# Performance work log

Hardware: AMD Instinct MI355X
Metric: run time of the kernel (lower is better)

## Reference

```python
import jax, jax.numpy as jnp
import numpy as np

B, C, FH, FW = 8, 256, 64, 64   # sketch/ref feature maps (B, C, F_H, F_W)
N = 131072                       # ~B*FH*FW*4 triplets, as the nested loops produce
MARGIN = 12.0


def setup_inputs() -> dict:
    key = jax.random.key(0)
    k1, k2, k3, k4, k5, k6 = jax.random.split(key, 6)
    sketch_query_vectors = jax.random.normal(k1, (B, C, FH, FW), jnp.float32)
    ref_key_vectors = jax.random.normal(k2, (B, C, FH, FW), jnp.float32)
    # Precomputed triplet indices. In the original these come from GridProcessing
    # (CPU grid math on G + random.choices negatives); they are constants w.r.t.
    # the float inputs, so we sample them once here.
    batch_idx = jax.random.randint(k3, (N,), 0, B, jnp.int32)
    anchor_yx = jax.random.randint(k4, (N, 2), 0, FH, jnp.int32)
    pos_yx = jax.random.randint(k5, (N, 2), 0, FH, jnp.int32)
    neg_yx = jax.random.randint(k6, (N, 2), 0, FH, jnp.int32)
    return {
        "sketch_query_vectors": sketch_query_vectors,
        "ref_key_vectors": ref_key_vectors,
        "batch_idx": batch_idx,
        "anchor_yx": anchor_yx,
        "pos_yx": pos_yx,
        "neg_yx": neg_yx,
    }


def reference(sketch_query_vectors, ref_key_vectors, batch_idx, anchor_yx, pos_yx, neg_yx):
    # Gather per-triplet feature vectors: [N, C]
    a = sketch_query_vectors[batch_idx, :, anchor_yx[:, 0], anchor_yx[:, 1]]
    p = ref_key_vectors[batch_idx, :, pos_yx[:, 0], pos_yx[:, 1]]
    n = ref_key_vectors[batch_idx, :, neg_yx[:, 0], neg_yx[:, 1]]
    dp = jnp.sum((a - p) ** 2, axis=-1)  # squared-euclidean, as calc_euclidean
    dn = jnp.sum((a - n) ** 2, axis=-1)
    losses = jax.nn.relu(dp - dn + MARGIN)  # per-triplet hinge (1-elem mean in orig)
    return jnp.sum(losses) / (1e-6 + N)
```

## Files before the change

### kernel.cpp

```cpp
#include <hip/hip_runtime.h>

#define NB 8
#define NC 256
#define FH 64
#define FW 64
#define NS (FH * FW)
#define NSAMP 131072
#define MARGIN_F 12.0f
#define GATHER_BLOCKS (NSAMP / 32)

typedef float vfloat2 __attribute__((ext_vector_type(2)));

__device__ __forceinline__ unsigned pack4_fp8(float f0, float f1, float f2, float f3)
{
    int r = __builtin_amdgcn_cvt_pk_fp8_f32(f0, f1, 0, false);
    r     = __builtin_amdgcn_cvt_pk_fp8_f32(f2, f3, r, true);
    return (unsigned)r;
}

__global__ __launch_bounds__(256) void transpose_to_bsc_fp8(
    const float* __restrict__ in0, const float* __restrict__ in1,
    unsigned char* __restrict__ out0, unsigned char* __restrict__ out1)
{
    __shared__ float tile[64][65];

    const int which = blockIdx.z >> 3;
    const int b     = blockIdx.z & 7;
    const float* __restrict__ in  = which ? in1 : in0;
    unsigned char* __restrict__ out = which ? out1 : out0;

    const int s0 = blockIdx.x * 64;
    const int c0 = blockIdx.y * 64;
    const int t  = threadIdx.x;

    const float* __restrict__ inb  = in  + (size_t)b * NC * NS;
    unsigned char* __restrict__ outb = out + (size_t)b * NS * NC;

    const int g   = t >> 4;
    const int sl4 = (t & 15) << 2;
#pragma unroll
    for (int pass = 0; pass < 4; ++pass) {
        const int cl = pass * 16 + g;
        const float4 v = *(const float4*)&inb[(size_t)(c0 + cl) * NS + (s0 + sl4)];
        tile[sl4 + 0][cl] = v.x;
        tile[sl4 + 1][cl] = v.y;
        tile[sl4 + 2][cl] = v.z;
        tile[sl4 + 3][cl] = v.w;
    }
    __syncthreads();

    const int cl4 = (t & 15) << 2;
#pragma unroll
    for (int pass = 0; pass < 4; ++pass) {
        const int sl = pass * 16 + (t >> 4);
        const unsigned w = pack4_fp8(tile[sl][cl4 + 0], tile[sl][cl4 + 1],
                                     tile[sl][cl4 + 2], tile[sl][cl4 + 3]);
        *(unsigned*)&outb[(size_t)(s0 + sl) * NC + (c0 + cl4)] = w;
    }
}

__device__ __forceinline__ void acc_u32(unsigned a, unsigned p, unsigned n, float& d)
{
    const vfloat2 a0 = __builtin_amdgcn_cvt_pk_f32_fp8(a, false);
    const vfloat2 a1 = __builtin_amdgcn_cvt_pk_f32_fp8(a, true);
    const vfloat2 p0 = __builtin_amdgcn_cvt_pk_f32_fp8(p, false);
    const vfloat2 p1 = __builtin_amdgcn_cvt_pk_f32_fp8(p, true);
    const vfloat2 n0 = __builtin_amdgcn_cvt_pk_f32_fp8(n, false);
    const vfloat2 n1 = __builtin_amdgcn_cvt_pk_f32_fp8(n, true);
    float t;
    t = a0.x - p0.x; d += t * t;  t = a0.x - n0.x; d -= t * t;
    t = a0.y - p0.y; d += t * t;  t = a0.y - n0.y; d -= t * t;
    t = a1.x - p1.x; d += t * t;  t = a1.x - n1.x; d -= t * t;
    t = a1.y - p1.y; d += t * t;  t = a1.y - n1.y; d -= t * t;
}

__device__ __forceinline__ void acc_quad(uint4 a, uint4 p, uint4 n, float& d)
{
    acc_u32(a.x, p.x, n.x, d);
    acc_u32(a.y, p.y, n.y, d);
    acc_u32(a.z, p.z, n.z, d);
    acc_u32(a.w, p.w, n.w, d);
}

__global__ __launch_bounds__(256) void triplet_gather_fp8(
    const uint4* __restrict__ tq,
    const uint4* __restrict__ tk,
    const int*  __restrict__ batch_idx,
    const int2* __restrict__ anchor_yx,
    const int2* __restrict__ pos_yx,
    const int2* __restrict__ neg_yx,
    float* __restrict__ partials)
{
    const int t    = threadIdx.x;
    const int ol   = t & 7;
    const int oct  = t >> 3;
    const int samp = blockIdx.x * 32 + oct;

    const int  b  = batch_idx[samp];
    const int2 ay = anchor_yx[samp];
    const int2 py = pos_yx[samp];
    const int2 ny = neg_yx[samp];

    const size_t ab = ((size_t)(b * NS) + ay.x * FW + ay.y) * 16;
    const size_t pb = ((size_t)(b * NS) + py.x * FW + py.y) * 16;
    const size_t nb = ((size_t)(b * NS) + ny.x * FW + ny.y) * 16;

    const uint4 A0 = tq[ab + ol];
    const uint4 A1 = tq[ab + 8 + ol];
    const uint4 P0 = tk[pb + ol];
    const uint4 P1 = tk[pb + 8 + ol];
    const uint4 N0 = tk[nb + ol];
    const uint4 N1 = tk[nb + 8 + ol];

    float d = 0.0f;
    acc_quad(A0, P0, N0, d);
    acc_quad(A1, P1, N1, d);

#pragma unroll
    for (int m = 1; m < 8; m <<= 1) d += __shfl_xor(d, m, 64);

    __shared__ float part[32];
    if (ol == 0) part[oct] = fmaxf(d + MARGIN_F, 0.0f);
    __syncthreads();
    if (t == 0) {
        float s = 0.0f;
#pragma unroll
        for (int i = 0; i < 32; ++i) s += part[i];
        partials[blockIdx.x] = s;
    }
}

__global__ __launch_bounds__(256) void final_reduce(
    const float* __restrict__ partials, float* __restrict__ out)
{
    float s = 0.0f;
    for (int i = threadIdx.x; i < GATHER_BLOCKS; i += 256) s += partials[i];
#pragma unroll
    for (int m = 1; m < 64; m <<= 1) s += __shfl_xor(s, m, 64);
    __shared__ float ws4[4];
    if ((threadIdx.x & 63) == 0) ws4[threadIdx.x >> 6] = s;
    __syncthreads();
    if (threadIdx.x == 0) {
        const float invN = 1.0f / (1e-6f + (float)NSAMP);
        out[0] = (ws4[0] + ws4[1] + ws4[2] + ws4[3]) * invN;
    }
}

__global__ __launch_bounds__(256) void triplet_direct(
    const float* __restrict__ q, const float* __restrict__ k,
    const int*  __restrict__ batch_idx,
    const int2* __restrict__ anchor_yx,
    const int2* __restrict__ pos_yx,
    const int2* __restrict__ neg_yx,
    float* __restrict__ out)
{
    const int lane   = threadIdx.x & 63;
    const int wid    = threadIdx.x >> 6;
    const int gwave  = blockIdx.x * 4 + wid;
    const int nwaves = gridDim.x * 4;

    float wsum = 0.0f;
    for (int i = gwave; i < NSAMP; i += nwaves) {
        const int  b  = batch_idx[i];
        const int2 ay = anchor_yx[i];
        const int2 py = pos_yx[i];
        const int2 ny = neg_yx[i];

        const size_t base = (size_t)b * NC * NS;
        const int sa = ay.x * FW + ay.y;
        const int sp = py.x * FW + py.y;
        const int sn = ny.x * FW + ny.y;

        float d = 0.0f;
#pragma unroll
        for (int kk = 0; kk < 4; ++kk) {
            const int c = lane + 64 * kk;
            const float av = q[base + (size_t)c * NS + sa];
            const float pv = k[base + (size_t)c * NS + sp];
            const float nv = k[base + (size_t)c * NS + sn];
            float t;
            t = av - pv; d += t * t;
            t = av - nv; d -= t * t;
        }
#pragma unroll
        for (int m = 1; m < 64; m <<= 1) d += __shfl_xor(d, m, 64);
        if (lane == 0) wsum += fmaxf(d + MARGIN_F, 0.0f);
    }

    __shared__ float bsum[4];
    if (lane == 0) bsum[wid] = wsum;
    __syncthreads();
    if (threadIdx.x == 0) {
        const float invN = 1.0f / (1e-6f + (float)NSAMP);
        atomicAdd(out, (bsum[0] + bsum[1] + bsum[2] + bsum[3]) * invN);
    }
}

extern "C" void kernel_launch(void* const* d_in, const int* in_sizes, int n_in,
                              void* d_out, int out_size, void* d_ws, size_t ws_size,
                              hipStream_t stream)
{
    const float* sketch = (const float*)d_in[0];
    const float* refk   = (const float*)d_in[1];
    const int*   bidx   = (const int*)d_in[2];
    const int2*  ayx    = (const int2*)d_in[3];
    const int2*  pyx    = (const int2*)d_in[4];
    const int2*  nyx    = (const int2*)d_in[5];
    float*       out    = (float*)d_out;

    const size_t tensor_elems = (size_t)NB * NC * NS;
    const size_t need = 2 * tensor_elems * sizeof(unsigned char)
                      + GATHER_BLOCKS * sizeof(float);

    if (ws_size >= need) {
        unsigned char* tq = (unsigned char*)d_ws;
        unsigned char* tk = tq + tensor_elems;
        float* partials = (float*)(tk + tensor_elems);

        dim3 tgrid(NS / 64, NC / 64, 16);
        transpose_to_bsc_fp8<<<tgrid, 256, 0, stream>>>(sketch, refk, tq, tk);

        triplet_gather_fp8<<<GATHER_BLOCKS, 256, 0, stream>>>(
            (const uint4*)tq, (const uint4*)tk, bidx, ayx, pyx, nyx, partials);

        final_reduce<<<1, 256, 0, stream>>>(partials, out);
    } else {
        (void)hipMemsetAsync(out, 0, sizeof(float), stream);
        triplet_direct<<<4096, 256, 0, stream>>>(
            sketch, refk, bidx, ayx, pyx, nyx, out);
    }
}
```

Baseline: 121.7 us.

## Bin gather samples by batch per block, flatten transpose grid, drop reduce kernel

The gather kernel now splits each window of 256 samples across 8 blocks. Each block is pinned to one batch index and compacts the samples of that batch with ballot and popcount, so every block touches only one batch slice of the fp8 tensors, which should improve L2 locality. The transpose is launched on a 1D grid with the batch index in the low bits, so concurrent blocks cover all batches, and it now writes 16-byte stores instead of 4-byte ones. The separate final reduce kernel is replaced by a memset plus a per-block atomicAdd. The cost is 8x more gather blocks, each reading the index array, uneven per-block work, and a float atomic sum whose order is not deterministic.

Result: slower. 165.6 us (+36.1%).

```diff
diff --git a/kernel.cpp b/kernel.cpp
--- a/kernel.cpp
+++ b/kernel.cpp
@@ -7,7 +7,8 @@
 #define NS (FH * FW)
 #define NSAMP 131072
 #define MARGIN_F 12.0f
-#define GATHER_BLOCKS (NSAMP / 32)
+#define NWIN (NSAMP / 256)
+#define GATHER_BLOCKS (NWIN * 8)
 
 typedef float vfloat2 __attribute__((ext_vector_type(2)));
 
@@ -24,16 +25,18 @@
 {
     __shared__ float tile[64][65];
 
-    const int which = blockIdx.z >> 3;
-    const int b     = blockIdx.z & 7;
+    const int bid    = blockIdx.x;
+    const int b      = bid & 7;
+    const int which  = (bid >> 3) & 1;
+    const int tile_i = bid >> 4;
+    const int s0     = (tile_i & 63) * 64;
+    const int c0     = (tile_i >> 6) * 64;
+    const int t      = threadIdx.x;
+
     const float* __restrict__ in  = which ? in1 : in0;
     unsigned char* __restrict__ out = which ? out1 : out0;
 
-    const int s0 = blockIdx.x * 64;
-    const int c0 = blockIdx.y * 64;
-    const int t  = threadIdx.x;
-
-    const float* __restrict__ inb  = in  + (size_t)b * NC * NS;
+    const float* __restrict__ inb   = in  + (size_t)b * NC * NS;
     unsigned char* __restrict__ outb = out + (size_t)b * NS * NC;
 
     const int g   = t >> 4;
@@ -49,14 +52,14 @@
     }
     __syncthreads();
 
-    const int cl4 = (t & 15) << 2;
-#pragma unroll
-    for (int pass = 0; pass < 4; ++pass) {
-        const int sl = pass * 16 + (t >> 4);
-        const unsigned w = pack4_fp8(tile[sl][cl4 + 0], tile[sl][cl4 + 1],
-                                     tile[sl][cl4 + 2], tile[sl][cl4 + 3]);
-        *(unsigned*)&outb[(size_t)(s0 + sl) * NC + (c0 + cl4)] = w;
-    }
+    const int sl = t >> 2;
+    const int cg = (t & 3) << 4;
+    uint4 w;
+    w.x = pack4_fp8(tile[sl][cg + 0],  tile[sl][cg + 1],  tile[sl][cg + 2],  tile[sl][cg + 3]);
+    w.y = pack4_fp8(tile[sl][cg + 4],  tile[sl][cg + 5],  tile[sl][cg + 6],  tile[sl][cg + 7]);
+    w.z = pack4_fp8(tile[sl][cg + 8],  tile[sl][cg + 9],  tile[sl][cg + 10], tile[sl][cg + 11]);
+    w.w = pack4_fp8(tile[sl][cg + 12], tile[sl][cg + 13], tile[sl][cg + 14], tile[sl][cg + 15]);
+    *(uint4*)&outb[(size_t)(s0 + sl) * NC + (c0 + cg)] = w;
 }
 
 __device__ __forceinline__ void acc_u32(unsigned a, unsigned p, unsigned n, float& d)
@@ -89,60 +92,76 @@
     const int2* __restrict__ anchor_yx,
     const int2* __restrict__ pos_yx,
     const int2* __restrict__ neg_yx,
-    float* __restrict__ partials)
+    float* __restrict__ out)
 {
     const int t    = threadIdx.x;
-    const int ol   = t & 7;
-    const int oct  = t >> 3;
-    const int samp = blockIdx.x * 32 + oct;
-
-    const int  b  = batch_idx[samp];
-    const int2 ay = anchor_yx[samp];
-    const int2 py = pos_yx[samp];
-    const int2 ny = neg_yx[samp];
-
-    const size_t ab = ((size_t)(b * NS) + ay.x * FW + ay.y) * 16;
-    const size_t pb = ((size_t)(b * NS) + py.x * FW + py.y) * 16;
-    const size_t nb = ((size_t)(b * NS) + ny.x * FW + ny.y) * 16;
-
-    const uint4 A0 = tq[ab + ol];
-    const uint4 A1 = tq[ab + 8 + ol];
-    const uint4 P0 = tk[pb + ol];
-    const uint4 P1 = tk[pb + 8 + ol];
-    const uint4 N0 = tk[nb + ol];
-    const uint4 N1 = tk[nb + 8 + ol];
-
-    float d = 0.0f;
-    acc_quad(A0, P0, N0, d);
-    acc_quad(A1, P1, N1, d);
-
-#pragma unroll
-    for (int m = 1; m < 8; m <<= 1) d += __shfl_xor(d, m, 64);
-
-    __shared__ float part[32];
-    if (ol == 0) part[oct] = fmaxf(d + MARGIN_F, 0.0f);
+    const int lane = t & 63;
+    const int wid  = t >> 6;
+    const int slot = blockIdx.x & 7;
+    const int win  = blockIdx.x >> 3;
+    const int s0   = win * 256;
+
+    __shared__ int   list[256];
+    __shared__ int   wtot[4];
+    __shared__ float bsum[4];
+
+    const int  b     = batch_idx[s0 + t];
+    const bool match = (b == slot);
+    const unsigned long long mask = __ballot(match);
+    if (lane == 0) wtot[wid] = (int)__popcll(mask);
+    __syncthreads();
+    int off = 0;
+#pragma unroll
+    for (int i = 0; i < 4; ++i) off += (i < wid) ? wtot[i] : 0;
+    const int count = wtot[0] + wtot[1] + wtot[2] + wtot[3];
+    if (match) {
+        const unsigned long long lt = (lane == 0) ? 0ull : ((1ull << lane) - 1ull);
+        list[off + (int)__popcll(mask & lt)] = t;
+    }
+    __syncthreads();
+
+    const int ol  = t & 7;
+    const int oct = t >> 3;
+    const size_t basebs = (size_t)slot * NS;
+    float acc = 0.0f;
+
+    for (int r = 0; r < count; r += 32) {
+        const int idx = r + oct;
+        if (idx < count) {
+            const int samp = s0 + list[idx];
+            const int2 ay = anchor_yx[samp];
+            const int2 py = pos_yx[samp];
+            const int2 ny = neg_yx[samp];
+
+            const size_t ab = (basebs + (size_t)(ay.x * FW + ay.y)) * 16;
+            const size_t pb = (basebs + (size_t)(py.x * FW + py.y)) * 16;
+            const size_t nb = (basebs + (size_t)(ny.x * FW + ny.y)) * 16;
+
+            const uint4 A0 = tq[ab + ol];
+            const uint4 A1 = tq[ab + 8 + ol];
+            const uint4 P0 = tk[pb + ol];
+            const uint4 P1 = tk[pb + 8 + ol];
+            const uint4 N0 = tk[nb + ol];
+            const uint4 N1 = tk[nb + 8 + ol];
+
+            float d = 0.0f;
+            acc_quad(A0, P0, N0, d);
+            acc_quad(A1, P1, N1, d);
+
+#pragma unroll
+            for (int m = 1; m < 8; m <<= 1) d += __shfl_xor(d, m, 64);
+            if (ol == 0) acc += fmaxf(d + MARGIN_F, 0.0f);
+        }
+    }
+
+    float s = acc;
+#pragma unroll
+    for (int m = 1; m < 64; m <<= 1) s += __shfl_xor(s, m, 64);
+    if (lane == 0) bsum[wid] = s;
     __syncthreads();
     if (t == 0) {
-        float s = 0.0f;
-#pragma unroll
-        for (int i = 0; i < 32; ++i) s += part[i];
-        partials[blockIdx.x] = s;
-    }
-}
-
-__global__ __launch_bounds__(256) void final_reduce(
-    const float* __restrict__ partials, float* __restrict__ out)
-{
-    float s = 0.0f;
-    for (int i = threadIdx.x; i < GATHER_BLOCKS; i += 256) s += partials[i];
-#pragma unroll
-    for (int m = 1; m < 64; m <<= 1) s += __shfl_xor(s, m, 64);
-    __shared__ float ws4[4];
-    if ((threadIdx.x & 63) == 0) ws4[threadIdx.x >> 6] = s;
-    __syncthreads();
-    if (threadIdx.x == 0) {
         const float invN = 1.0f / (1e-6f + (float)NSAMP);
-        out[0] = (ws4[0] + ws4[1] + ws4[2] + ws4[3]) * invN;
+        atomicAdd(out, (bsum[0] + bsum[1] + bsum[2] + bsum[3]) * invN);
     }
 }
 
@@ -209,23 +228,19 @@
     float*       out    = (float*)d_out;
 
     const size_t tensor_elems = (size_t)NB * NC * NS;
-    const size_t need = 2 * tensor_elems * sizeof(unsigned char)
-                      + GATHER_BLOCKS * sizeof(float);
+    const size_t need = 2 * tensor_elems * sizeof(unsigned char);
+
+    (void)hipMemsetAsync(out, 0, sizeof(float), stream);
 
     if (ws_size >= need) {
         unsigned char* tq = (unsigned char*)d_ws;
         unsigned char* tk = tq + tensor_elems;
-        float* partials = (float*)(tk + tensor_elems);
-
-        dim3 tgrid(NS / 64, NC / 64, 16);
-        transpose_to_bsc_fp8<<<tgrid, 256, 0, stream>>>(sketch, refk, tq, tk);
+
+        transpose_to_bsc_fp8<<<4096, 256, 0, stream>>>(sketch, refk, tq, tk);
 
         triplet_gather_fp8<<<GATHER_BLOCKS, 256, 0, stream>>>(
-            (const uint4*)tq, (const uint4*)tk, bidx, ayx, pyx, nyx, partials);
-
-        final_reduce<<<1, 256, 0, stream>>>(partials, out);
+            (const uint4*)tq, (const uint4*)tk, bidx, ayx, pyx, nyx, out);
     } else {
-        (void)hipMemsetAsync(out, 0, sizeof(float), stream);
         triplet_direct<<<4096, 256, 0, stream>>>(
             sketch, refk, bidx, ayx, pyx, nyx, out);
     }
```
